# Kernel tuning notes

Hardware: AMD Instinct MI355X
Metric: run time of the kernel (lower is better)

Reference implementation:

```python
import jax, jax.numpy as jnp
import numpy as np

HEADS = 12
FEATURES = 768
D_HEAD = FEATURES // HEADS
SCALE = float(np.sqrt(D_HEAD))
EPS = 1e-12
N = 2048


def setup_inputs() -> dict:
    key = jax.random.key(0)
    ks = jax.random.split(key, 5)
    init = 1.0 / np.sqrt(FEATURES)
    return {
        "x": jax.random.normal(ks[0], (N, FEATURES), dtype=jnp.float32),
        "Wq": jax.random.normal(ks[1], (FEATURES, FEATURES), dtype=jnp.float32) * init,
        "Wk": jax.random.normal(ks[2], (FEATURES, FEATURES), dtype=jnp.float32) * init,
        "Wv": jax.random.normal(ks[3], (FEATURES, FEATURES), dtype=jnp.float32) * init,
        "Wo": jax.random.normal(ks[4], (FEATURES, FEATURES), dtype=jnp.float32) * init,
        "gamma": jnp.ones((FEATURES,), dtype=jnp.float32),
        "beta": jnp.zeros((FEATURES,), dtype=jnp.float32),
    }


def reference(x, Wq, Wk, Wv, Wo, gamma, beta):
    n = x.shape[0]
    # projections (no bias); weight layout [out, in] -> x @ W.T
    q = (x @ Wq.T).reshape(n, HEADS, D_HEAD).transpose(1, 0, 2)  # [h, n, d]
    k = (x @ Wk.T).reshape(n, HEADS, D_HEAD).transpose(1, 0, 2)
    v = (x @ Wv.T).reshape(n, HEADS, D_HEAD).transpose(1, 0, 2)
    # scores [h, n, n]; original divides q@k^T by sqrt(d_head)
    att = jnp.einsum("hnd,hmd->hnm", q, k) / SCALE
    att = jax.nn.softmax(att, axis=-1)  # dropout p=0 -> identity
    out = jnp.einsum("hnm,hmd->hnd", att, v)  # [h, n, d]
    out = out.transpose(1, 0, 2).reshape(n, FEATURES)  # n (h d)
    out = out @ Wo.T
    # residual + layernorm (eps=1e-12)
    y = out + x
    mu = jnp.mean(y, axis=-1, keepdims=True)
    var = jnp.mean((y - mu) ** 2, axis=-1, keepdims=True)
    return (y - mu) / jnp.sqrt(var + EPS) * gamma + beta
```

## Files before the change

### kernel.cpp

```cpp
#include <hip/hip_runtime.h>
#include <hip/hip_bf16.h>
#include <math.h>

#define N_TOK 2048
#define FEAT  768
#define HEADS 12
#define DHEAD 64
#define SPLIT 4
#define KV_PER (N_TOK / SPLIT)

typedef __bf16 v8bf __attribute__((ext_vector_type(8)));
typedef __bf16 v4bf __attribute__((ext_vector_type(4)));
typedef float  v4f  __attribute__((ext_vector_type(4)));

#define XE ((size_t)N_TOK * FEAT)
#define QK_LD 1536

#define SCALE_FOLD 0.18033688011112042f

__device__ __forceinline__ void gload16(const __bf16* g, __bf16* l) {
    __builtin_amdgcn_global_load_lds(
        (const __attribute__((address_space(1))) unsigned int*)g,
        (__attribute__((address_space(3))) unsigned int*)l, 16, 0, 0);
}

__global__ __launch_bounds__(256) void gemm_qkv(
        const float* __restrict__ x,  const float* __restrict__ Wq,
        const float* __restrict__ Wk, const float* __restrict__ Wv,
        __bf16* __restrict__ qk, __bf16* __restrict__ vt) {
    __shared__ __bf16 As[64][32];
    __shared__ __bf16 Bs[128][32];
    const int t    = threadIdx.x;
    const int lane = t & 63, w = t >> 6;
    const int quad = lane >> 4, l15 = lane & 15;
    const int wm = w & 1, wn = w >> 1;
    const int bm = blockIdx.y * 64, bn = blockIdx.x * 128;

    const float* Bsrc; float scale = 1.f; int bc0 = bn;
    if (bn < FEAT)            { Bsrc = Wq; scale = SCALE_FOLD; }
    else if (bn < 2 * FEAT)   { Bsrc = Wk; bc0 = bn - FEAT; }
    else                      { Bsrc = Wv; bc0 = bn - 2 * FEAT; }

    const int ar = t >> 2, ac = (t & 3) * 8;
    const int br = t >> 1, bc = (t & 1) * 16;

    v4f acc[2][4] = {};
    for (int k0 = 0; k0 < FEAT; k0 += 32) {
        {
            const float* ap = x + (size_t)(bm + ar) * FEAT + k0 + ac;
            float4 a0 = *(const float4*)ap, a1 = *(const float4*)(ap + 4);
            v8bf av;
            av[0]=(__bf16)a0.x; av[1]=(__bf16)a0.y; av[2]=(__bf16)a0.z; av[3]=(__bf16)a0.w;
            av[4]=(__bf16)a1.x; av[5]=(__bf16)a1.y; av[6]=(__bf16)a1.z; av[7]=(__bf16)a1.w;
            *(v8bf*)&As[ar][ac] = av;
        }
        {
            const float* bp = Bsrc + (size_t)(bc0 + br) * FEAT + k0 + bc;
            float4 b0 = *(const float4*)bp,     b1 = *(const float4*)(bp + 4);
            float4 b2 = *(const float4*)(bp+8), b3 = *(const float4*)(bp + 12);
            v8bf v0, v1;
            v0[0]=(__bf16)(b0.x*scale); v0[1]=(__bf16)(b0.y*scale); v0[2]=(__bf16)(b0.z*scale); v0[3]=(__bf16)(b0.w*scale);
            v0[4]=(__bf16)(b1.x*scale); v0[5]=(__bf16)(b1.y*scale); v0[6]=(__bf16)(b1.z*scale); v0[7]=(__bf16)(b1.w*scale);
            v1[0]=(__bf16)(b2.x*scale); v1[1]=(__bf16)(b2.y*scale); v1[2]=(__bf16)(b2.z*scale); v1[3]=(__bf16)(b2.w*scale);
            v1[4]=(__bf16)(b3.x*scale); v1[5]=(__bf16)(b3.y*scale); v1[6]=(__bf16)(b3.z*scale); v1[7]=(__bf16)(b3.w*scale);
            *(v8bf*)&Bs[br][bc]     = v0;
            *(v8bf*)&Bs[br][bc + 8] = v1;
        }
        __syncthreads();
        v8bf a[2], b[4];
#pragma unroll
        for (int mi = 0; mi < 2; mi++) a[mi] = *(const v8bf*)&As[wm * 32 + mi * 16 + l15][quad * 8];
#pragma unroll
        for (int ni = 0; ni < 4; ni++) b[ni] = *(const v8bf*)&Bs[wn * 64 + ni * 16 + l15][quad * 8];
#pragma unroll
        for (int mi = 0; mi < 2; mi++)
#pragma unroll
            for (int ni = 0; ni < 4; ni++)
                acc[mi][ni] = __builtin_amdgcn_mfma_f32_16x16x32_bf16(a[mi], b[ni], acc[mi][ni], 0, 0, 0);
        __syncthreads();
    }
    if (bn < 2 * FEAT) {
#pragma unroll
        for (int mi = 0; mi < 2; mi++)
#pragma unroll
            for (int ni = 0; ni < 4; ni++) {
                int col = bn + wn * 64 + ni * 16 + l15;
#pragma unroll
                for (int r = 0; r < 4; r++) {
                    int row = bm + wm * 32 + mi * 16 + quad * 4 + r;
                    qk[(size_t)row * QK_LD + col] = (__bf16)acc[mi][ni][r];
                }
            }
    } else {
#pragma unroll
        for (int mi = 0; mi < 2; mi++)
#pragma unroll
            for (int ni = 0; ni < 4; ni++) {
                int col = bn + wn * 64 + ni * 16 + l15 - 2 * FEAT;
                int row = bm + wm * 32 + mi * 16 + quad * 4;
                v4bf pk;
#pragma unroll
                for (int r = 0; r < 4; r++) pk[r] = (__bf16)acc[mi][ni][r];
                *(v4bf*)(vt + (size_t)col * N_TOK + row) = pk;
            }
    }
}

__global__ __launch_bounds__(256, 3) void attention(
        const __bf16* __restrict__ QK, const __bf16* __restrict__ vt,
        __bf16* __restrict__ Opart, float* __restrict__ lpart) {
    __shared__ __bf16 KV[2][2][64][64];
    __shared__ __bf16 P[4][32][68];
    const int t    = threadIdx.x;
    const int lane = t & 63, w = t >> 6;
    const int quad = lane >> 4, l15 = lane & 15;
    const int h = blockIdx.y, s = blockIdx.z;
    const int q0 = blockIdx.x * 128 + w * 32;

    v8bf qf[2][2];
#pragma unroll
    for (int mh = 0; mh < 2; mh++) {
        const __bf16* qp = QK + (size_t)(q0 + mh * 16 + l15) * QK_LD + h * DHEAD + quad * 8;
        qf[mh][0] = *(const v8bf*)qp;
        qf[mh][1] = *(const v8bf*)(qp + 32);
    }
    const __bf16* kg = QK + FEAT + h * DHEAD;
    const __bf16* vg = vt + (size_t)(h * DHEAD) * N_TOK;

    v4f o_acc[2][4] = {};
    float lacc[2][4] = {{0.f,0.f,0.f,0.f},{0.f,0.f,0.f,0.f}};

    const int kvbeg = s * KV_PER;
    const int lr8 = lane >> 3;

    auto stage = [&](int b, int kv0) {
#pragma unroll
        for (int i = 0; i < 2; i++) {
            int row = w * 16 + i * 8 + lr8;
            int gs  = (lane & 7) ^ (row & 7);
            gload16(kg + (size_t)(kv0 + row) * QK_LD + gs * 8, &KV[b][0][w * 16 + i * 8][0]);
            gload16(vg + (size_t)row * N_TOK + kv0 + gs * 8,   &KV[b][1][w * 16 + i * 8][0]);
        }
    };

    auto step = [&](int b) {
        v8bf kf[4][2];
#pragma unroll
        for (int nt = 0; nt < 4; nt++)
#pragma unroll
            for (int ks = 0; ks < 2; ks++)
                kf[nt][ks] = *(const v8bf*)&KV[b][0][nt * 16 + l15][((ks * 4 + quad) ^ (l15 & 7)) * 8];
        v4f sv[2][4];
#pragma unroll
        for (int mh = 0; mh < 2; mh++)
#pragma unroll
            for (int nt = 0; nt < 4; nt++) {
                v4f a = {};
                a = __builtin_amdgcn_mfma_f32_16x16x32_bf16(qf[mh][0], kf[nt][0], a, 0, 0, 0);
                a = __builtin_amdgcn_mfma_f32_16x16x32_bf16(qf[mh][1], kf[nt][1], a, 0, 0, 0);
                sv[mh][nt] = a;
            }
#pragma unroll
        for (int mh = 0; mh < 2; mh++)
#pragma unroll
            for (int r = 0; r < 4; r++) {
                float p0 = __builtin_amdgcn_exp2f(sv[mh][0][r]);
                float p1 = __builtin_amdgcn_exp2f(sv[mh][1][r]);
                float p2 = __builtin_amdgcn_exp2f(sv[mh][2][r]);
                float p3 = __builtin_amdgcn_exp2f(sv[mh][3][r]);
                lacc[mh][r] += (p0 + p1) + (p2 + p3);
                P[w][mh * 16 + quad * 4 + r][ 0 + l15] = (__bf16)p0;
                P[w][mh * 16 + quad * 4 + r][16 + l15] = (__bf16)p1;
                P[w][mh * 16 + quad * 4 + r][32 + l15] = (__bf16)p2;
                P[w][mh * 16 + quad * 4 + r][48 + l15] = (__bf16)p3;
            }
        v8bf vf[2][4];
#pragma unroll
        for (int ks = 0; ks < 2; ks++)
#pragma unroll
            for (int dt = 0; dt < 4; dt++)
                vf[ks][dt] = *(const v8bf*)&KV[b][1][dt * 16 + l15][((ks * 4 + quad) ^ (l15 & 7)) * 8];
#pragma unroll
        for (int mh = 0; mh < 2; mh++)
#pragma unroll
            for (int ks = 0; ks < 2; ks++) {
                v8bf pa = *(const v8bf*)&P[w][mh * 16 + l15][ks * 32 + quad * 8];
#pragma unroll
                for (int dt = 0; dt < 4; dt++)
                    o_acc[mh][dt] = __builtin_amdgcn_mfma_f32_16x16x32_bf16(pa, vf[ks][dt], o_acc[mh][dt], 0, 0, 0);
            }
    };

    stage(0, kvbeg);
    const int TILES = KV_PER / 64;
    for (int tt = 0; tt < TILES; tt++) {
        __syncthreads();
        if (tt + 1 < TILES) stage((tt + 1) & 1, kvbeg + (tt + 1) * 64);
        step(tt & 1);
    }

    __bf16* op = Opart + (size_t)s * XE;
#pragma unroll
    for (int mh = 0; mh < 2; mh++)
#pragma unroll
        for (int r = 0; r < 4; r++) {
            float l = lacc[mh][r];
            l += __shfl_xor(l, 1); l += __shfl_xor(l, 2);
            l += __shfl_xor(l, 4); l += __shfl_xor(l, 8);
            float linv = 1.0f / l;
            int row = q0 + mh * 16 + quad * 4 + r;
            if (l15 == 0) lpart[((size_t)s * HEADS + h) * N_TOK + row] = l;
#pragma unroll
            for (int dt = 0; dt < 4; dt++)
                op[(size_t)row * FEAT + h * DHEAD + dt * 16 + l15] = (__bf16)(o_acc[mh][dt][r] * linv);
        }
}

__global__ __launch_bounds__(256) void gemm_out(
        const __bf16* __restrict__ Op, const float* __restrict__ lp,
        const float* __restrict__ Wo,  const float* __restrict__ x,
        float* __restrict__ Yf) {
    __shared__ __bf16 As[64][32];
    __shared__ __bf16 Bs[128][32];
    const int t    = threadIdx.x;
    const int lane = t & 63, w = t >> 6;
    const int quad = lane >> 4, l15 = lane & 15;
    const int wm = w & 1, wn = w >> 1;
    const int bm = blockIdx.y * 64, bn = blockIdx.x * 128;

    const int ar = t >> 2, ac = (t & 3) * 8;
    const int br = t >> 1, bc = (t & 1) * 16;
    const int arow = bm + ar;

    v4f acc[2][4] = {};
    for (int k0 = 0; k0 < FEAT; k0 += 32) {
        {
            int h = (k0 + ac) >> 6;
            float ls[SPLIT], tot = 0.f;
#pragma unroll
            for (int s = 0; s < SPLIT; s++) {
                ls[s] = lp[((size_t)s * HEADS + h) * N_TOK + arow];
                tot += ls[s];
            }
            float inv = 1.0f / tot;
            float a8[8] = {};
#pragma unroll
            for (int s = 0; s < SPLIT; s++) {
                v8bf p = *(const v8bf*)(Op + (size_t)s * XE + (size_t)arow * FEAT + k0 + ac);
                float wgt = ls[s] * inv;
#pragma unroll
                for (int j = 0; j < 8; j++) a8[j] += wgt * (float)p[j];
            }
            v8bf av;
#pragma unroll
            for (int j = 0; j < 8; j++) av[j] = (__bf16)a8[j];
            *(v8bf*)&As[ar][ac] = av;
        }
        {
            const float* bp = Wo + (size_t)(bn + br) * FEAT + k0 + bc;
            float4 b0 = *(const float4*)bp,     b1 = *(const float4*)(bp + 4);
            float4 b2 = *(const float4*)(bp+8), b3 = *(const float4*)(bp + 12);
            v8bf v0, v1;
            v0[0]=(__bf16)b0.x; v0[1]=(__bf16)b0.y; v0[2]=(__bf16)b0.z; v0[3]=(__bf16)b0.w;
            v0[4]=(__bf16)b1.x; v0[5]=(__bf16)b1.y; v0[6]=(__bf16)b1.z; v0[7]=(__bf16)b1.w;
            v1[0]=(__bf16)b2.x; v1[1]=(__bf16)b2.y; v1[2]=(__bf16)b2.z; v1[3]=(__bf16)b2.w;
            v1[4]=(__bf16)b3.x; v1[5]=(__bf16)b3.y; v1[6]=(__bf16)b3.z; v1[7]=(__bf16)b3.w;
            *(v8bf*)&Bs[br][bc]     = v0;
            *(v8bf*)&Bs[br][bc + 8] = v1;
        }
        __syncthreads();
        v8bf a[2], b[4];
#pragma unroll
        for (int mi = 0; mi < 2; mi++) a[mi] = *(const v8bf*)&As[wm * 32 + mi * 16 + l15][quad * 8];
#pragma unroll
        for (int ni = 0; ni < 4; ni++) b[ni] = *(const v8bf*)&Bs[wn * 64 + ni * 16 + l15][quad * 8];
#pragma unroll
        for (int mi = 0; mi < 2; mi++)
#pragma unroll
            for (int ni = 0; ni < 4; ni++)
                acc[mi][ni] = __builtin_amdgcn_mfma_f32_16x16x32_bf16(a[mi], b[ni], acc[mi][ni], 0, 0, 0);
        __syncthreads();
    }
#pragma unroll
    for (int mi = 0; mi < 2; mi++)
#pragma unroll
        for (int ni = 0; ni < 4; ni++) {
            int col = bn + wn * 64 + ni * 16 + l15;
#pragma unroll
            for (int r = 0; r < 4; r++) {
                int row = bm + wm * 32 + mi * 16 + quad * 4 + r;
                Yf[(size_t)row * FEAT + col] = acc[mi][ni][r] + x[(size_t)row * FEAT + col];
            }
        }
}

__global__ __launch_bounds__(256) void ln_kernel(
        const float* __restrict__ Y, const float* __restrict__ gamma,
        const float* __restrict__ beta, float* __restrict__ out) {
    __shared__ float sbuf[4];
    const int row = blockIdx.x, t = threadIdx.x;
    const float* y = Y + (size_t)row * FEAT;
    float v0 = y[t], v1 = y[t + 256], v2 = y[t + 512];
    float s = v0 + v1 + v2;
#pragma unroll
    for (int m = 32; m; m >>= 1) s += __shfl_xor(s, m);
    if ((t & 63) == 0) sbuf[t >> 6] = s;
    __syncthreads();
    float mean = (sbuf[0] + sbuf[1] + sbuf[2] + sbuf[3]) * (1.f / FEAT);
    __syncthreads();
    float d0 = v0 - mean, d1 = v1 - mean, d2 = v2 - mean;
    float q = d0 * d0 + d1 * d1 + d2 * d2;
#pragma unroll
    for (int m = 32; m; m >>= 1) q += __shfl_xor(q, m);
    if ((t & 63) == 0) sbuf[t >> 6] = q;
    __syncthreads();
    float var = (sbuf[0] + sbuf[1] + sbuf[2] + sbuf[3]) * (1.f / FEAT);
    float rs = rsqrtf(var + 1e-12f);
    float* o = out + (size_t)row * FEAT;
    o[t]       = d0 * rs * gamma[t]       + beta[t];
    o[t + 256] = d1 * rs * gamma[t + 256] + beta[t + 256];
    o[t + 512] = d2 * rs * gamma[t + 512] + beta[t + 512];
}

extern "C" void kernel_launch(void* const* d_in, const int* in_sizes, int n_in,
                              void* d_out, int out_size, void* d_ws, size_t ws_size,
                              hipStream_t stream) {
    const float* x     = (const float*)d_in[0];
    const float* Wq    = (const float*)d_in[1];
    const float* Wk    = (const float*)d_in[2];
    const float* Wv    = (const float*)d_in[3];
    const float* Wo    = (const float*)d_in[4];
    const float* gamma = (const float*)d_in[5];
    const float* beta  = (const float*)d_in[6];
    float* out = (float*)d_out;

    char* ws = (char*)d_ws;
    size_t off = 0;
    auto alloc = [&](size_t bytes) -> void* {
        void* p = ws + off;
        off += (bytes + 255) & ~(size_t)255;
        return p;
    };
    __bf16* qk  = (__bf16*)alloc((size_t)N_TOK * QK_LD * 2);
    __bf16* vtb = (__bf16*)alloc((size_t)FEAT * N_TOK * 2);
    __bf16* Op  = (__bf16*)alloc(SPLIT * XE * 2);
    float*  lp  = (float*)alloc(SPLIT * HEADS * N_TOK * 4);
    float*  Yf  = (float*)ws;

    gemm_qkv<<<dim3((QK_LD + FEAT) / 128, N_TOK / 64), 256, 0, stream>>>(
        x, Wq, Wk, Wv, qk, vtb);

    attention<<<dim3(N_TOK / 128, HEADS, SPLIT), 256, 0, stream>>>(qk, vtb, Op, lp);

    gemm_out<<<dim3(FEAT / 128, N_TOK / 64), 256, 0, stream>>>(Op, lp, Wo, x, Yf);

    ln_kernel<<<N_TOK, 256, 0, stream>>>(Yf, gamma, beta, out);
}
```

Before: 158.2 us.

## Pre-convert inputs and weights to bf16 and stream GEMM tiles into LDS

Adds a conversion kernel that turns x, Wq, Wk, Wv and Wo from fp32 to bf16 once per call, folding the softmax scale into Wq. The QKV and output GEMMs then load bf16 tiles with global_load_lds directly into shared memory. This removes the repeated fp32 loads and register conversions that every GEMM tile did before. It costs an extra launch and an extra pass over the inputs through workspace memory.

```diff
diff --git a/kernel.cpp b/kernel.cpp
--- a/kernel.cpp
+++ b/kernel.cpp
@@ -14,6 +14,7 @@
 typedef float  v4f  __attribute__((ext_vector_type(4)));
 
 #define XE ((size_t)N_TOK * FEAT)
+#define WE ((size_t)FEAT * FEAT)
 #define QK_LD 1536
 
 #define SCALE_FOLD 0.18033688011112042f
@@ -24,9 +25,27 @@
         (__attribute__((address_space(3))) unsigned int*)l, 16, 0, 0);
 }
 
-__global__ __launch_bounds__(256) void gemm_qkv(
+__global__ __launch_bounds__(256) void cvt_all(
         const float* __restrict__ x,  const float* __restrict__ Wq,
         const float* __restrict__ Wk, const float* __restrict__ Wv,
+        const float* __restrict__ Wo,
+        __bf16* __restrict__ xb, __bf16* __restrict__ wqkv, __bf16* __restrict__ wob) {
+    size_t i = ((size_t)blockIdx.x * 256 + threadIdx.x) * 4;
+    const float* src; __bf16* dst; size_t off; float scale = 1.f;
+    if (i < XE)               { src = x;  dst = xb;          off = i; }
+    else if (i < XE + WE)     { src = Wq; dst = wqkv;        off = i - XE; scale = SCALE_FOLD; }
+    else if (i < XE + 2 * WE) { src = Wk; dst = wqkv + WE;   off = i - XE - WE; }
+    else if (i < XE + 3 * WE) { src = Wv; dst = wqkv + 2*WE; off = i - XE - 2*WE; }
+    else                      { src = Wo; dst = wob;         off = i - XE - 3*WE; }
+    float4 v = *(const float4*)(src + off);
+    v4bf o;
+    o[0] = (__bf16)(v.x * scale); o[1] = (__bf16)(v.y * scale);
+    o[2] = (__bf16)(v.z * scale); o[3] = (__bf16)(v.w * scale);
+    *(v4bf*)(dst + off) = o;
+}
+
+__global__ __launch_bounds__(256) void gemm_qkv(
+        const __bf16* __restrict__ A, const __bf16* __restrict__ B,
         __bf16* __restrict__ qk, __bf16* __restrict__ vt) {
     __shared__ __bf16 As[64][32];
     __shared__ __bf16 Bs[128][32];
@@ -35,37 +54,13 @@
     const int quad = lane >> 4, l15 = lane & 15;
     const int wm = w & 1, wn = w >> 1;
     const int bm = blockIdx.y * 64, bn = blockIdx.x * 128;
-
-    const float* Bsrc; float scale = 1.f; int bc0 = bn;
-    if (bn < FEAT)            { Bsrc = Wq; scale = SCALE_FOLD; }
-    else if (bn < 2 * FEAT)   { Bsrc = Wk; bc0 = bn - FEAT; }
-    else                      { Bsrc = Wv; bc0 = bn - 2 * FEAT; }
-
-    const int ar = t >> 2, ac = (t & 3) * 8;
-    const int br = t >> 1, bc = (t & 1) * 16;
+    const int srow = lane >> 2, scol = (lane & 3) * 8;
 
     v4f acc[2][4] = {};
     for (int k0 = 0; k0 < FEAT; k0 += 32) {
-        {
-            const float* ap = x + (size_t)(bm + ar) * FEAT + k0 + ac;
-            float4 a0 = *(const float4*)ap, a1 = *(const float4*)(ap + 4);
-            v8bf av;
-            av[0]=(__bf16)a0.x; av[1]=(__bf16)a0.y; av[2]=(__bf16)a0.z; av[3]=(__bf16)a0.w;
-            av[4]=(__bf16)a1.x; av[5]=(__bf16)a1.y; av[6]=(__bf16)a1.z; av[7]=(__bf16)a1.w;
-            *(v8bf*)&As[ar][ac] = av;
-        }
-        {
-            const float* bp = Bsrc + (size_t)(bc0 + br) * FEAT + k0 + bc;
-            float4 b0 = *(const float4*)bp,     b1 = *(const float4*)(bp + 4);
-            float4 b2 = *(const float4*)(bp+8), b3 = *(const float4*)(bp + 12);
-            v8bf v0, v1;
-            v0[0]=(__bf16)(b0.x*scale); v0[1]=(__bf16)(b0.y*scale); v0[2]=(__bf16)(b0.z*scale); v0[3]=(__bf16)(b0.w*scale);
-            v0[4]=(__bf16)(b1.x*scale); v0[5]=(__bf16)(b1.y*scale); v0[6]=(__bf16)(b1.z*scale); v0[7]=(__bf16)(b1.w*scale);
-            v1[0]=(__bf16)(b2.x*scale); v1[1]=(__bf16)(b2.y*scale); v1[2]=(__bf16)(b2.z*scale); v1[3]=(__bf16)(b2.w*scale);
-            v1[4]=(__bf16)(b3.x*scale); v1[5]=(__bf16)(b3.y*scale); v1[6]=(__bf16)(b3.z*scale); v1[7]=(__bf16)(b3.w*scale);
-            *(v8bf*)&Bs[br][bc]     = v0;
-            *(v8bf*)&Bs[br][bc + 8] = v1;
-        }
+        gload16(A + (size_t)(bm + w * 16 + srow) * FEAT + k0 + scol,      &As[w * 16][0]);
+        gload16(B + (size_t)(bn + w * 32 + srow) * FEAT + k0 + scol,      &Bs[w * 32][0]);
+        gload16(B + (size_t)(bn + w * 32 + 16 + srow) * FEAT + k0 + scol, &Bs[w * 32 + 16][0]);
         __syncthreads();
         v8bf a[2], b[4];
 #pragma unroll
@@ -218,7 +213,7 @@
 
 __global__ __launch_bounds__(256) void gemm_out(
         const __bf16* __restrict__ Op, const float* __restrict__ lp,
-        const float* __restrict__ Wo,  const float* __restrict__ x,
+        const __bf16* __restrict__ Wo, const float* __restrict__ x,
         float* __restrict__ Yf) {
     __shared__ __bf16 As[64][32];
     __shared__ __bf16 Bs[128][32];
@@ -227,9 +222,9 @@
     const int quad = lane >> 4, l15 = lane & 15;
     const int wm = w & 1, wn = w >> 1;
     const int bm = blockIdx.y * 64, bn = blockIdx.x * 128;
+    const int srow = lane >> 2, scol = (lane & 3) * 8;
 
     const int ar = t >> 2, ac = (t & 3) * 8;
-    const int br = t >> 1, bc = (t & 1) * 16;
     const int arow = bm + ar;
 
     v4f acc[2][4] = {};
@@ -256,18 +251,8 @@
             for (int j = 0; j < 8; j++) av[j] = (__bf16)a8[j];
             *(v8bf*)&As[ar][ac] = av;
         }
-        {
-            const float* bp = Wo + (size_t)(bn + br) * FEAT + k0 + bc;
-            float4 b0 = *(const float4*)bp,     b1 = *(const float4*)(bp + 4);
-            float4 b2 = *(const float4*)(bp+8), b3 = *(const float4*)(bp + 12);
-            v8bf v0, v1;
-            v0[0]=(__bf16)b0.x; v0[1]=(__bf16)b0.y; v0[2]=(__bf16)b0.z; v0[3]=(__bf16)b0.w;
-            v0[4]=(__bf16)b1.x; v0[5]=(__bf16)b1.y; v0[6]=(__bf16)b1.z; v0[7]=(__bf16)b1.w;
-            v1[0]=(__bf16)b2.x; v1[1]=(__bf16)b2.y; v1[2]=(__bf16)b2.z; v1[3]=(__bf16)b2.w;
-            v1[4]=(__bf16)b3.x; v1[5]=(__bf16)b3.y; v1[6]=(__bf16)b3.z; v1[7]=(__bf16)b3.w;
-            *(v8bf*)&Bs[br][bc]     = v0;
-            *(v8bf*)&Bs[br][bc + 8] = v1;
-        }
+        gload16(Wo + (size_t)(bn + w * 32 + srow) * FEAT + k0 + scol,      &Bs[w * 32][0]);
+        gload16(Wo + (size_t)(bn + w * 32 + 16 + srow) * FEAT + k0 + scol, &Bs[w * 32 + 16][0]);
         __syncthreads();
         v8bf a[2], b[4];
 #pragma unroll
@@ -341,18 +326,22 @@
         off += (bytes + 255) & ~(size_t)255;
         return p;
     };
-    __bf16* qk  = (__bf16*)alloc((size_t)N_TOK * QK_LD * 2);
-    __bf16* vtb = (__bf16*)alloc((size_t)FEAT * N_TOK * 2);
-    __bf16* Op  = (__bf16*)alloc(SPLIT * XE * 2);
-    float*  lp  = (float*)alloc(SPLIT * HEADS * N_TOK * 4);
-    float*  Yf  = (float*)ws;
-
-    gemm_qkv<<<dim3((QK_LD + FEAT) / 128, N_TOK / 64), 256, 0, stream>>>(
-        x, Wq, Wk, Wv, qk, vtb);
+    __bf16* xb   = (__bf16*)alloc(XE * 2);
+    __bf16* wqkv = (__bf16*)alloc(3 * WE * 2);
+    __bf16* wob  = (__bf16*)alloc(WE * 2);
+    __bf16* qk   = (__bf16*)alloc((size_t)N_TOK * QK_LD * 2);
+    __bf16* vtb  = (__bf16*)alloc((size_t)FEAT * N_TOK * 2);
+    __bf16* Op   = (__bf16*)alloc(SPLIT * XE * 2);
+    float*  lp   = (float*)alloc(SPLIT * HEADS * N_TOK * 4);
+    float*  Yf   = (float*)ws;
+
+    cvt_all<<<(int)((XE + 4 * WE) / 4 / 256), 256, 0, stream>>>(x, Wq, Wk, Wv, Wo, xb, wqkv, wob);
+
+    gemm_qkv<<<dim3((QK_LD + FEAT) / 128, N_TOK / 64), 256, 0, stream>>>(xb, wqkv, qk, vtb);
 
     attention<<<dim3(N_TOK / 128, HEADS, SPLIT), 256, 0, stream>>>(qk, vtb, Op, lp);
 
-    gemm_out<<<dim3(FEAT / 128, N_TOK / 64), 256, 0, stream>>>(Op, lp, Wo, x, Yf);
+    gemm_out<<<dim3(FEAT / 128, N_TOK / 64), 256, 0, stream>>>(Op, lp, wob, x, Yf);
 
     ln_kernel<<<N_TOK, 256, 0, stream>>>(Yf, gamma, beta, out);
 }
```

New measurement: 151.2 us. -4.4%, faster.
